# Optimization experiments

Measured on AMD Instinct MI355X. Metric: run time of the kernel, lower is better.

## Reference

```python
import jax, jax.numpy as jnp
import numpy as np

N, H, E = 16384, 1024, 8


def setup_inputs() -> dict:
    key = jax.random.key(0)
    ks = jax.random.split(key, 6)
    scale = 0.02
    tokens = jax.random.normal(ks[0], (N, H), dtype=jnp.float32)
    gate_w = jax.random.normal(ks[1], (E, H), dtype=jnp.float32) * scale  # torch Linear weight [out,in]
    w1 = jax.random.normal(ks[2], (E, H, H), dtype=jnp.float32) * scale   # per-expert first Linear [out,in]
    b1 = jax.random.normal(ks[3], (E, H), dtype=jnp.float32) * scale
    w2 = jax.random.normal(ks[4], (E, H, H), dtype=jnp.float32) * scale   # per-expert second Linear [out,in]
    b2 = jax.random.normal(ks[5], (E, H), dtype=jnp.float32) * scale
    return {"tokens": tokens, "gate_w": gate_w, "w1": w1, "b1": b1, "w2": w2, "b2": b2}


def reference(tokens, gate_w, w1, b1, w2, b2):
    # gate: logits [N,E], top-1 routing (output is NOT scaled by gate weight, matching the torch module)
    logits = jnp.einsum('nh,eh->ne', tokens, gate_w)
    weights = jax.nn.softmax(logits, axis=-1)
    top1 = jnp.argmax(weights, axis=-1)                     # [N] int
    onehot = jax.nn.one_hot(top1, w1.shape[0], dtype=tokens.dtype)  # [N,E]
    out = jnp.zeros_like(tokens)
    for e in range(w1.shape[0]):  # small fixed expert count
        h = jax.nn.relu(jnp.einsum('nh,fh->nf', tokens, w1[e]) + b1[e])
        y = jnp.einsum('nf,gf->ng', h, w2[e]) + b2[e]
        out = out + onehot[:, e:e + 1] * y
    return out
```

## Files before the change

### kernel.cpp

```cpp
#include <hip/hip_runtime.h>
#include <hip/hip_bf16.h>
#include <stdint.h>

#define N_TOK 16384
#define HDIM  1024
#define NE    8

#define BM 128
#define BN 128
#define BK 64
#define NKT (HDIM / BK)
#define NT_N (HDIM / BN)
#define MAXTILES (N_TOK / BM + NE)
#define GRID_GEMM (MAXTILES * NT_N)

typedef __attribute__((ext_vector_type(8))) short          bf16x8;
typedef __attribute__((ext_vector_type(8))) unsigned short ushort8;
typedef __attribute__((ext_vector_type(4))) unsigned short ushort4v;
typedef __attribute__((ext_vector_type(4))) float          f32x4;

__device__ __forceinline__ unsigned short f2bf(float f) {
  union { float f; uint32_t u; } c; c.f = f;
  uint32_t u = c.u;
  uint32_t r = (u + 0x7fffu + ((u >> 16) & 1u)) >> 16;
  return (unsigned short)r;
}

__device__ __forceinline__ void gload_lds16(const void* g, void* l) {
  __builtin_amdgcn_global_load_lds((const __attribute__((address_space(1))) void*)g,
                                   (__attribute__((address_space(3))) void*)l, 16, 0, 0);
}

__device__ __forceinline__ void expert_range(const int* __restrict__ counts, int e,
                                             int& base, int& cnt) {
  int run = 0; base = 0; cnt = 0;
#pragma unroll
  for (int i = 0; i < NE; ++i) {
    int c = counts[i];
    if (i == e) { base = run; cnt = c; }
    run += c;
  }
}

__global__ __launch_bounds__(256) void gate_kernel(
    const float* __restrict__ tokens, const float* __restrict__ gate_w,
    const float* __restrict__ w1f, const float* __restrict__ w2f,
    unsigned short* __restrict__ tokB, unsigned short* __restrict__ w1B,
    unsigned short* __restrict__ w2B, int* __restrict__ eid)
{
  int wid  = threadIdx.x >> 6;
  int lane = threadIdx.x & 63;
  int n    = blockIdx.x * 4 + wid;

  const float* trow = tokens + (size_t)n * HDIM;
  float4 x[4];
#pragma unroll
  for (int i = 0; i < 4; ++i)
    x[i] = *(const float4*)(trow + i * 256 + lane * 4);

  unsigned short* drow = tokB + (size_t)n * HDIM;
#pragma unroll
  for (int i = 0; i < 4; ++i) {
    ushort4v o;
    o[0] = f2bf(x[i].x); o[1] = f2bf(x[i].y);
    o[2] = f2bf(x[i].z); o[3] = f2bf(x[i].w);
    *(ushort4v*)(drow + i * 256 + lane * 4) = o;
  }

  double acc[NE];
#pragma unroll
  for (int e = 0; e < NE; ++e) {
    const float* grow = gate_w + e * HDIM;
    double a = 0.0;
#pragma unroll
    for (int i = 0; i < 4; ++i) {
      float4 g = *(const float4*)(grow + i * 256 + lane * 4);
      a += (double)x[i].x * g.x + (double)x[i].y * g.y
         + (double)x[i].z * g.z + (double)x[i].w * g.w;
    }
    acc[e] = a;
  }
#pragma unroll
  for (int off = 32; off; off >>= 1) {
#pragma unroll
    for (int e = 0; e < NE; ++e) acc[e] += __shfl_xor(acc[e], off);
  }
  if (lane == 0) {
    int best = 0; double bv = acc[0];
#pragma unroll
    for (int e = 1; e < NE; ++e) if (acc[e] > bv) { bv = acc[e]; best = e; }
    eid[n] = best;
  }

  {
    int b = blockIdx.x;
    const float* src = (b < 2048) ? w1f : w2f;
    unsigned short* dst = (b < 2048) ? w1B : w2B;
    size_t i0 = ((size_t)(b & 2047) * 4096) + (size_t)threadIdx.x * 16;
#pragma unroll
    for (int h = 0; h < 2; ++h) {
      float4 fa = *(const float4*)(src + i0 + h * 8);
      float4 fb = *(const float4*)(src + i0 + h * 8 + 4);
      ushort8 o;
      o[0] = f2bf(fa.x); o[1] = f2bf(fa.y); o[2] = f2bf(fa.z); o[3] = f2bf(fa.w);
      o[4] = f2bf(fb.x); o[5] = f2bf(fb.y); o[6] = f2bf(fb.z); o[7] = f2bf(fb.w);
      *(ushort8*)(dst + i0 + h * 8) = o;
    }
  }
}

__global__ __launch_bounds__(256) void rank_kernel(
    const int* __restrict__ eid, int* __restrict__ rank, int* __restrict__ counts)
{
  __shared__ int h[NE];
  __shared__ int bbase[NE];
  int t = threadIdx.x;
  int n = blockIdx.x * 256 + t;
  if (t < NE) h[t] = 0;
  __syncthreads();
  int e = eid[n];
  int r = atomicAdd(&h[e], 1);
  __syncthreads();
  if (t < NE) bbase[t] = atomicAdd(&counts[t], h[t]);
  __syncthreads();
  rank[n] = bbase[e] + r;
}

__global__ __launch_bounds__(256) void perm_kernel(
    const int* __restrict__ counts, const int* __restrict__ eid,
    const int* __restrict__ rank, int* __restrict__ topos,
    int* __restrict__ tmeta)
{
  __shared__ int off[NE];
  int t = threadIdx.x;
  if (t == 0) {
    int run = 0;
#pragma unroll
    for (int e = 0; e < NE; ++e) { off[e] = run; run += counts[e]; }
  }
  __syncthreads();
  int n = blockIdx.x * 256 + t;
  topos[off[eid[n]] + rank[n]] = n;
  if (blockIdx.x == 0 && t == 0) {
    int idx = 0;
    for (int e = 0; e < NE; ++e) {
      int ntile = (counts[e] + BM - 1) / BM;
      for (int mt = 0; mt < ntile; ++mt) tmeta[1 + idx++] = (mt << 3) | e;
    }
    tmeta[0] = idx;
  }
}

#define GEMM_PREAMBLE()                                                        \
  int bid = blockIdx.x;                                                        \
  int logical = (bid & 7) * (GRID_GEMM / 8) + (bid >> 3);                      \
  int tile = logical >> 3;                                                     \
  int nt   = logical & 7;                                                      \
  if (tile >= tmeta[0]) return;                                                \
  int ent = tmeta[1 + tile];                                                   \
  int e = ent & 7, mt = ent >> 3;                                              \
  int base, cnt;                                                               \
  expert_range(counts, e, base, cnt);                                          \
  __shared__ unsigned short Alds[BM * BK];                                     \
  __shared__ unsigned short Blds[BN * BK];                                     \
  int t    = threadIdx.x;                                                      \
  int kc   = t & 7;                                  \
  int rowi = t >> 3;                                                \
  int sch  = kc ^ (rowi & 7);               \
  int lane = t & 63, wid = t >> 6;                                             \
  int wr = wid >> 1, wc = wid & 1;                                             \
  f32x4 acc[4][4] = {};                                                        \
  int arow0 = wr * 64 + (lane & 15);                                           \
  int brow0 = wc * 64 + (lane & 15);                                           \
  int hi    = lane >> 4;                                             \
  int xo    = lane & 7;

#define GEMM_STAGE(kt)                                                         \
  _Pragma("unroll")                                                            \
  for (int r = 0; r < 4; ++r) {                                                \
    gload_lds16(APTR(r, kt), Alds + t * 8 + 2048 * r);                         \
    gload_lds16(bsrc + (size_t)(kt) * BK + (size_t)(32 * r) * HDIM,            \
                Blds + t * 8 + 2048 * r);                                      \
  }

#define GEMM_COMPUTE()                                                         \
  _Pragma("unroll")                                                            \
  for (int ks = 0; ks < 2; ++ks) {                                             \
    int ch = ((ks * 4 + hi) ^ xo) * 8;                                         \
    bf16x8 af[4], bv[4];                                                       \
    _Pragma("unroll")                                                          \
    for (int m = 0; m < 4; ++m)                                                \
      af[m] = *(const bf16x8*)(Alds + (arow0 + m * 16) * BK + ch);             \
    _Pragma("unroll")                                                          \
    for (int n2 = 0; n2 < 4; ++n2)                                             \
      bv[n2] = *(const bf16x8*)(Blds + (brow0 + n2 * 16) * BK + ch);           \
    _Pragma("unroll")                                                          \
    for (int m = 0; m < 4; ++m)                                                \
      _Pragma("unroll")                                                        \
      for (int n2 = 0; n2 < 4; ++n2)                                           \
        acc[m][n2] = __builtin_amdgcn_mfma_f32_16x16x32_bf16(                  \
            af[m], bv[n2], acc[m][n2], 0, 0, 0);                               \
  }

#define GEMM_MAINLOOP()                                                        \
  for (int kt = 0; kt < NKT; ++kt) {                                           \
    __syncthreads();                                                           \
    GEMM_STAGE(kt);                                                            \
    __syncthreads();                                                           \
    GEMM_COMPUTE();                                                            \
  }

__global__ __launch_bounds__(256) void gemm1_kernel(
    const unsigned short* __restrict__ tokB,
    const unsigned short* __restrict__ w1B,
    const float* __restrict__ b1,
    const int* __restrict__ counts,
    const int* __restrict__ tmeta,
    const int* __restrict__ topos,
    unsigned short* __restrict__ Hbuf)
{
  GEMM_PREAMBLE()
  int tokr[4];
#pragma unroll
  for (int r = 0; r < 4; ++r) {
    int pos = base + mt * BM + rowi + 32 * r;
    if (pos > N_TOK - 1) pos = N_TOK - 1;
    tokr[r] = topos[pos];
  }
  const unsigned short* bsrc =
      w1B + ((size_t)e << 20) + (size_t)(nt * BN + rowi) * HDIM + sch * 8;
#define APTR(r, kt) (tokB + (size_t)tokr[r] * HDIM + (kt) * BK + sch * 8)
  GEMM_MAINLOOP()
#undef APTR

  int crow0 = wr * 64 + (lane >> 4) * 4;
  int ccol0 = wc * 64 + (lane & 15);
  float bias[4];
#pragma unroll
  for (int n2 = 0; n2 < 4; ++n2)
    bias[n2] = b1[e * HDIM + nt * BN + ccol0 + n2 * 16];
#pragma unroll
  for (int m = 0; m < 4; ++m) {
#pragma unroll
    for (int j = 0; j < 4; ++j) {
      int row = crow0 + m * 16 + j;
      if (mt * BM + row < cnt) {
        size_t orow = (size_t)(base + mt * BM + row) * HDIM + nt * BN;
#pragma unroll
        for (int n2 = 0; n2 < 4; ++n2) {
          float v = acc[m][n2][j] + bias[n2];
          v = v > 0.f ? v : 0.f;
          Hbuf[orow + ccol0 + n2 * 16] = f2bf(v);
        }
      }
    }
  }
}

__global__ __launch_bounds__(256) void gemm2_kernel(
    const unsigned short* __restrict__ Hbuf,
    const unsigned short* __restrict__ w2B,
    const float* __restrict__ b2,
    const int* __restrict__ counts,
    const int* __restrict__ tmeta,
    const int* __restrict__ topos,
    float* __restrict__ out)
{
  GEMM_PREAMBLE()
  int arows[4];
#pragma unroll
  for (int r = 0; r < 4; ++r) {
    int pos = base + mt * BM + rowi + 32 * r;
    arows[r] = pos > N_TOK - 1 ? N_TOK - 1 : pos;
  }
  const unsigned short* bsrc =
      w2B + ((size_t)e << 20) + (size_t)(nt * BN + rowi) * HDIM + sch * 8;
#define APTR(r, kt) (Hbuf + (size_t)arows[r] * HDIM + (kt) * BK + sch * 8)
  GEMM_MAINLOOP()
#undef APTR

  int crow0 = wr * 64 + (lane >> 4) * 4;
  int ccol0 = wc * 64 + (lane & 15);
  float bias[4];
#pragma unroll
  for (int n2 = 0; n2 < 4; ++n2)
    bias[n2] = b2[e * HDIM + nt * BN + ccol0 + n2 * 16];
#pragma unroll
  for (int m = 0; m < 4; ++m) {
#pragma unroll
    for (int j = 0; j < 4; ++j) {
      int row = crow0 + m * 16 + j;
      if (mt * BM + row < cnt) {
        int tok = topos[base + mt * BM + row];
        size_t orow = (size_t)tok * HDIM + nt * BN;
#pragma unroll
        for (int n2 = 0; n2 < 4; ++n2)
          out[orow + ccol0 + n2 * 16] = acc[m][n2][j] + bias[n2];
      }
    }
  }
}

extern "C" void kernel_launch(void* const* d_in, const int* in_sizes, int n_in,
                              void* d_out, int out_size, void* d_ws, size_t ws_size,
                              hipStream_t stream) {
  (void)in_sizes; (void)n_in; (void)out_size; (void)ws_size;
  const float* tokens = (const float*)d_in[0];
  const float* gate_w = (const float*)d_in[1];
  const float* w1     = (const float*)d_in[2];
  const float* b1     = (const float*)d_in[3];
  const float* w2     = (const float*)d_in[4];
  const float* b2     = (const float*)d_in[5];
  float* out          = (float*)d_out;

  char* ws = (char*)d_ws;
  size_t o = 0;
  int* counts = (int*)(ws + o); o += 256;
  int* tmeta  = (int*)(ws + o); o += 1024;
  int* eid    = (int*)(ws + o); o += (size_t)N_TOK * 4;
  int* rank   = (int*)(ws + o); o += (size_t)N_TOK * 4;
  int* topos  = (int*)(ws + o); o += (size_t)N_TOK * 4;
  unsigned short* tokB = (unsigned short*)(ws + o); o += (size_t)N_TOK * HDIM * 2;
  unsigned short* w1B  = (unsigned short*)(ws + o); o += (size_t)NE * HDIM * HDIM * 2;
  unsigned short* w2B  = (unsigned short*)(ws + o); o += (size_t)NE * HDIM * HDIM * 2;
  unsigned short* Hbuf = (unsigned short*)(ws + o); o += (size_t)N_TOK * HDIM * 2;

  hipMemsetAsync(counts, 0, 64, stream);
  gate_kernel<<<N_TOK / 4, 256, 0, stream>>>(tokens, gate_w, w1, w2,
                                             tokB, w1B, w2B, eid);
  rank_kernel<<<N_TOK / 256, 256, 0, stream>>>(eid, rank, counts);
  perm_kernel<<<N_TOK / 256, 256, 0, stream>>>(counts, eid, rank, topos, tmeta);
  gemm1_kernel<<<GRID_GEMM, 256, 0, stream>>>(tokB, w1B, b1, counts, tmeta, topos, Hbuf);
  gemm2_kernel<<<GRID_GEMM, 256, 0, stream>>>(Hbuf, w2B, b2, counts, tmeta, topos, out);
}
```

Baseline: 170.6 us.

## Move w2 fp32-to-bf16 conversion into gemm1 blocks to overlap with compute

The w2 weight conversion moves out of the gate kernel and into the first 1024 blocks of gemm1, where it runs before those blocks start their GEMM tile. The gate kernel grows extra blocks that convert only w1, at 32 elements per thread instead of 16. The aim is to take 32 MB of w2 traffic off the gate kernel's critical path and hide it under gemm1's compute. In exchange, the first gemm1 blocks get longer and may delay the tail, and some gemm1 blocks that early-exit still do conversion work.

Result: slower. 175.2 us (+2.7%).

```diff
diff --git a/kernel.cpp b/kernel.cpp
--- a/kernel.cpp
+++ b/kernel.cpp
@@ -42,12 +42,30 @@
   }
 }
 
+__device__ __forceinline__ void cvt_slice(const float* __restrict__ src,
+                                          unsigned short* __restrict__ dst,
+                                          int sliceIdx, int tid) {
+  size_t i0 = (size_t)sliceIdx * 8192 + (size_t)tid * 32;
+#pragma unroll
+  for (int h = 0; h < 4; ++h) {
+    float4 fa = *(const float4*)(src + i0 + h * 8);
+    float4 fb = *(const float4*)(src + i0 + h * 8 + 4);
+    ushort8 o;
+    o[0] = f2bf(fa.x); o[1] = f2bf(fa.y); o[2] = f2bf(fa.z); o[3] = f2bf(fa.w);
+    o[4] = f2bf(fb.x); o[5] = f2bf(fb.y); o[6] = f2bf(fb.z); o[7] = f2bf(fb.w);
+    *(ushort8*)(dst + i0 + h * 8) = o;
+  }
+}
+
 __global__ __launch_bounds__(256) void gate_kernel(
     const float* __restrict__ tokens, const float* __restrict__ gate_w,
-    const float* __restrict__ w1f, const float* __restrict__ w2f,
-    unsigned short* __restrict__ tokB, unsigned short* __restrict__ w1B,
-    unsigned short* __restrict__ w2B, int* __restrict__ eid)
-{
+    const float* __restrict__ w1f, unsigned short* __restrict__ w1B,
+    unsigned short* __restrict__ tokB, int* __restrict__ eid)
+{
+  if (blockIdx.x >= 4096) {
+    cvt_slice(w1f, w1B, blockIdx.x - 4096, threadIdx.x);
+    return;
+  }
   int wid  = threadIdx.x >> 6;
   int lane = threadIdx.x & 63;
   int n    = blockIdx.x * 4 + wid;
@@ -90,22 +108,6 @@
 #pragma unroll
     for (int e = 1; e < NE; ++e) if (acc[e] > bv) { bv = acc[e]; best = e; }
     eid[n] = best;
-  }
-
-  {
-    int b = blockIdx.x;
-    const float* src = (b < 2048) ? w1f : w2f;
-    unsigned short* dst = (b < 2048) ? w1B : w2B;
-    size_t i0 = ((size_t)(b & 2047) * 4096) + (size_t)threadIdx.x * 16;
-#pragma unroll
-    for (int h = 0; h < 2; ++h) {
-      float4 fa = *(const float4*)(src + i0 + h * 8);
-      float4 fb = *(const float4*)(src + i0 + h * 8 + 4);
-      ushort8 o;
-      o[0] = f2bf(fa.x); o[1] = f2bf(fa.y); o[2] = f2bf(fa.z); o[3] = f2bf(fa.w);
-      o[4] = f2bf(fb.x); o[5] = f2bf(fb.y); o[6] = f2bf(fb.z); o[7] = f2bf(fb.w);
-      *(ushort8*)(dst + i0 + h * 8) = o;
-    }
   }
 }
 
@@ -152,7 +154,6 @@
 }
 
 #define GEMM_PREAMBLE()                                                        \
-  int bid = blockIdx.x;                                                        \
   int logical = (bid & 7) * (GRID_GEMM / 8) + (bid >> 3);                      \
   int tile = logical >> 3;                                                     \
   int nt   = logical & 7;                                                      \
@@ -214,11 +215,16 @@
     const unsigned short* __restrict__ tokB,
     const unsigned short* __restrict__ w1B,
     const float* __restrict__ b1,
+    const float* __restrict__ w2f,
+    unsigned short* __restrict__ w2B,
     const int* __restrict__ counts,
     const int* __restrict__ tmeta,
     const int* __restrict__ topos,
     unsigned short* __restrict__ Hbuf)
 {
+  int bid = blockIdx.x;
+  if (bid < 1024) cvt_slice(w2f, w2B, bid, threadIdx.x);
+
   GEMM_PREAMBLE()
   int tokr[4];
 #pragma unroll
@@ -266,6 +272,7 @@
     const int* __restrict__ topos,
     float* __restrict__ out)
 {
+  int bid = blockIdx.x;
   GEMM_PREAMBLE()
   int arows[4];
 #pragma unroll
@@ -326,10 +333,10 @@
   unsigned short* Hbuf = (unsigned short*)(ws + o); o += (size_t)N_TOK * HDIM * 2;
 
   hipMemsetAsync(counts, 0, 64, stream);
-  gate_kernel<<<N_TOK / 4, 256, 0, stream>>>(tokens, gate_w, w1, w2,
-                                             tokB, w1B, w2B, eid);
+  gate_kernel<<<5120, 256, 0, stream>>>(tokens, gate_w, w1, w1B, tokB, eid);
   rank_kernel<<<N_TOK / 256, 256, 0, stream>>>(eid, rank, counts);
   perm_kernel<<<N_TOK / 256, 256, 0, stream>>>(counts, eid, rank, topos, tmeta);
-  gemm1_kernel<<<GRID_GEMM, 256, 0, stream>>>(tokB, w1B, b1, counts, tmeta, topos, Hbuf);
+  gemm1_kernel<<<GRID_GEMM, 256, 0, stream>>>(tokB, w1B, b1, w2, w2B,
+                                              counts, tmeta, topos, Hbuf);
   gemm2_kernel<<<GRID_GEMM, 256, 0, stream>>>(Hbuf, w2B, b2, counts, tmeta, topos, out);
 }
```
